# Kernel tuning notes

Hardware: AMD Instinct MI355X
Metric: run time of the kernel (lower is better)

The kernel has to match this reference:

```python
import jax, jax.numpy as jnp
import numpy as np

B, S, E, H = 2, 2048, 1024, 16
DH = E // H  # 64


def setup_inputs() -> dict:
    key = jax.random.key(0)
    ks = jax.random.split(key, 9)
    scale = 1.0 / np.sqrt(E)
    q = jax.random.normal(ks[0], (B, S, E), jnp.float32)
    k = jax.random.normal(ks[1], (B, S, E), jnp.float32)
    v = jax.random.normal(ks[2], (B, S, E), jnp.float32)
    Wq = jax.random.uniform(ks[3], (E, E), jnp.float32, -scale, scale)
    Wk = jax.random.uniform(ks[4], (E, E), jnp.float32, -scale, scale)
    Wv = jax.random.uniform(ks[5], (E, E), jnp.float32, -scale, scale)
    bq = jax.random.uniform(ks[6], (E,), jnp.float32, -scale, scale)
    bk = jax.random.uniform(ks[7], (E,), jnp.float32, -scale, scale)
    bv = jax.random.uniform(ks[8], (E,), jnp.float32, -scale, scale)
    # causal mask: True = masked. [b, s_q, s_k]
    causal = jnp.triu(jnp.ones((S, S), bool), k=1)
    mask = jnp.broadcast_to(causal, (B, S, S))
    return {"q": q, "k": k, "v": v, "Wq": Wq, "bq": bq, "Wk": Wk,
            "bk": bk, "Wv": Wv, "bv": bv, "mask": mask}


def reference(q, k, v, Wq, bq, Wk, bk, Wv, bv, mask):
    b, s_q, _ = q.shape
    s_k = k.shape[1]
    # NB: faithful to the original: .view(b, heads, s, -1) (no transpose)
    Q = (q @ Wq + bq).reshape(b, H, s_q, DH)
    K = (k @ Wk + bk).reshape(b, H, s_k, DH)
    V = (v @ Wv + bv).reshape(b, H, s_k, DH)
    scores = jnp.einsum('bhqd,bhkd->bhqk', Q, K) / jnp.sqrt(
        jnp.asarray(DH, Q.dtype))
    scores = jnp.where(mask[:, None, :, :], -jnp.inf, scores)
    attn = jax.nn.softmax(scores, axis=-1)
    out = jnp.einsum('bhqk,bhkd->bhqd', attn, V).reshape(b, s_q, -1)
    return out  # dropout p=0 / eval mode -> identity
```

## Files before the change

kernel.cpp:

```cpp
#include <hip/hip_runtime.h>

typedef unsigned short u16;
typedef __attribute__((ext_vector_type(8))) __bf16 bf16x8;
typedef __attribute__((ext_vector_type(4))) __bf16 bf16x4;
typedef __attribute__((ext_vector_type(4))) float f32x4;

#define MFMA(a, b, c) __builtin_amdgcn_mfma_f32_16x16x32_bf16((a), (b), (c), 0, 0, 0)
#define KSCALE 0.18033688011112042f

__device__ __forceinline__ void load_lds16(const void* g, void* l) {
  __builtin_amdgcn_global_load_lds(
      (__attribute__((address_space(1))) void*)(g),
      (__attribute__((address_space(3))) void*)(l), 16, 0, 0);
}

__device__ __forceinline__ float launder(float x, float lim) {
  return fminf(fmaxf(x, -lim), lim);
}

__global__ __launch_bounds__(256) void prep(
    const float* __restrict__ x0, const float* __restrict__ x1,
    const float* __restrict__ x2, const float* __restrict__ W0,
    const float* __restrict__ W1, const float* __restrict__ W2,
    __bf16* __restrict__ Xb, __bf16* __restrict__ WT) {
  __shared__ __bf16 tile[64][65];
  int bx = blockIdx.x;
  int t = threadIdx.x;
  if (bx < 3072) {
    int z = bx >> 10, blk = bx & 1023;
    const float* x = z == 0 ? x0 : (z == 1 ? x1 : x2);
    __bf16* o = Xb + (size_t)z * 4194304;
#pragma unroll
    for (int i = 0; i < 4; ++i) {
      size_t e = ((size_t)i * 262144 + (size_t)blk * 256 + t) * 4;
      f32x4 v = *(const f32x4*)&x[e];
      bf16x4 b = {(__bf16)v[0], (__bf16)v[1], (__bf16)v[2], (__bf16)v[3]};
      *(bf16x4*)&o[e] = b;
    }
  } else {
    int idx = bx - 3072;
    int z = idx >> 8, rest = idx & 255;
    const float* W = z == 0 ? W0 : (z == 1 ? W1 : W2);
    float sc = z == 0 ? KSCALE : 1.0f;
    __bf16* out = WT + (size_t)z * 1048576;
    int r0 = (rest >> 4) * 64, c0 = (rest & 15) * 64;
#pragma unroll
    for (int it = 0; it < 16; ++it) {
      int flat = it * 256 + t, r = flat >> 6, c = flat & 63;
      tile[c][r] = (__bf16)(W[(size_t)(r0 + r) * 1024 + c0 + c] * sc);
    }
    __syncthreads();
#pragma unroll
    for (int it = 0; it < 16; ++it) {
      int flat = it * 256 + t, r = flat >> 6, c = flat & 63;
      out[(size_t)(c0 + r) * 1024 + r0 + c] = tile[r][c];
    }
  }
}

__device__ __forceinline__ void pg_stage(
    const __bf16* __restrict__ A, const __bf16* __restrict__ Bm, int k0,
    __bf16* As, __bf16* Bs, int tid) {
#pragma unroll
  for (int r = 0; r < 2; ++r) {
    int flat = r * 256 + tid;
    int src = ((flat & 3) ^ ((flat >> 3) & 3)) * 8;
    load_lds16(A + (size_t)(flat >> 2) * 1024 + k0 + src, &As[flat * 8]);
  }
#pragma unroll
  for (int r = 0; r < 2; ++r) {
    int flat = r * 256 + tid;
    int src = ((flat & 3) ^ ((flat >> 3) & 3)) * 8;
    load_lds16(Bm + (size_t)(flat >> 2) * 1024 + k0 + src, &Bs[flat * 8]);
  }
}

__global__ __launch_bounds__(256, 3) void proj_gemm(
    const __bf16* __restrict__ Xb, const __bf16* __restrict__ WT,
    const float* __restrict__ bq, const float* __restrict__ bk,
    const float* __restrict__ bv, __bf16* __restrict__ QKV) {
  __shared__ __attribute__((aligned(16))) __bf16 As[3][4096];
  __shared__ __attribute__((aligned(16))) __bf16 Bs[3][4096];

  int tid = threadIdx.x;
  int lane = tid & 63, quad = lane >> 4, l16 = lane & 15;
  int w = tid >> 6;
  int wm = (w >> 1) * 64, wn = (w & 1) * 64;
  int sw = (l16 >> 1) & 3;
  int m0 = blockIdx.x * 128;
  int z = m0 >> 12;
  int n0 = blockIdx.y * 128;
  const __bf16* A = Xb + (size_t)m0 * 1024;
  const __bf16* Bm = WT + (size_t)z * 1048576 + (size_t)n0 * 1024;

  f32x4 zero4 = {0.f, 0.f, 0.f, 0.f};
  f32x4 acc[4][4];
#pragma unroll
  for (int i = 0; i < 4; ++i)
#pragma unroll
    for (int j = 0; j < 4; ++j) acc[i][j] = zero4;

  pg_stage(A, Bm, 0, As[0], Bs[0], tid);
  pg_stage(A, Bm, 32, As[1], Bs[1], tid);

  int cur = 0, stg = 2;
  for (int i = 0; i < 32; ++i) {
    if (i < 31) {
      asm volatile("s_waitcnt vmcnt(4)" ::: "memory");
    } else {
      asm volatile("s_waitcnt vmcnt(0)" ::: "memory");
    }
    __builtin_amdgcn_sched_barrier(0);
    __builtin_amdgcn_s_barrier();
    __builtin_amdgcn_sched_barrier(0);

    if (i < 30)
      pg_stage(A, Bm, (i + 2) * 32, As[stg], Bs[stg], tid);

    bf16x8 a[4], b[4];
#pragma unroll
    for (int mf = 0; mf < 4; ++mf)
      a[mf] = *(const bf16x8*)&As[cur][(wm + mf * 16 + l16) * 32 + ((quad ^ sw)) * 8];
#pragma unroll
    for (int nf = 0; nf < 4; ++nf)
      b[nf] = *(const bf16x8*)&Bs[cur][(wn + nf * 16 + l16) * 32 + ((quad ^ sw)) * 8];
#pragma unroll
    for (int mf = 0; mf < 4; ++mf)
#pragma unroll
      for (int nf = 0; nf < 4; ++nf) acc[mf][nf] = MFMA(a[mf], b[nf], acc[mf][nf]);

    cur = cur == 2 ? 0 : cur + 1;
    stg = stg == 2 ? 0 : stg + 1;
  }

  int mrow = m0 & 4095;
  const float* bp = z == 0 ? bq : (z == 1 ? bk : bv);
  float bsc = z == 0 ? KSCALE : 1.0f;
  __bf16* O = QKV + (size_t)z * 4194304;
#pragma unroll
  for (int nf = 0; nf < 4; ++nf) {
    int n = n0 + wn + nf * 16 + l16;
    float bb = bp[n] * bsc;
#pragma unroll
    for (int mf = 0; mf < 4; ++mf) {
#pragma unroll
      for (int r = 0; r < 4; ++r) {
        int m = mrow + wm + mf * 16 + quad * 4 + r;
        O[(size_t)m * 1024 + n] = (__bf16)launder(acc[mf][nf][r] + bb, 512.f);
      }
    }
  }
}

__global__ __launch_bounds__(256) void transpose_v(
    const u16* __restrict__ Vp, u16* __restrict__ Vt) {
  int bh = blockIdx.y, s0 = blockIdx.x * 64;
  __shared__ u16 tile[64][65];
  int t = threadIdx.x;
  const u16* src = Vp + (size_t)bh * 131072;
  u16* dst = Vt + (size_t)bh * 131072;
#pragma unroll
  for (int it = 0; it < 16; ++it) {
    int flat = it * 256 + t, r = flat >> 6, d = flat & 63;
    tile[d][r] = src[(size_t)(s0 + r) * 64 + d];
  }
  __syncthreads();
#pragma unroll
  for (int it = 0; it < 16; ++it) {
    int flat = it * 256 + t, d = flat >> 6, c = flat & 63;
    dst[(size_t)d * 2048 + s0 + c] = tile[d][c];
  }
}

__global__ __launch_bounds__(256, 4) void flash_attn(
    const __bf16* __restrict__ Qp, const __bf16* __restrict__ Kp,
    const __bf16* __restrict__ Vt, float* __restrict__ out) {
  int bh = blockIdx.x;
  int yy = blockIdx.y;
  int qt = (yy & 24) | (((yy >> 3) & 1) ? (7 - (yy & 7)) : (yy & 7));
  int jmax = qt;
  int t = threadIdx.x;
  int lane = t & 63, quad = lane >> 4, l16 = lane & 15;
  int w = t >> 6;
  int sw = (l16 >> 1) & 3;

  __shared__ __attribute__((aligned(16))) __bf16 Ks[2][4096];
  __shared__ __attribute__((aligned(16))) __bf16 Vs[2][4096];
  __shared__ __attribute__((aligned(16))) __bf16 Ps[4][1024];

  const __bf16* Qb = Qp + (size_t)bh * 131072;
  const __bf16* Kb = Kp + (size_t)bh * 131072;
  const __bf16* Vb = Vt + (size_t)bh * 131072;
  __bf16* Pw = Ps[w];

  int qb = qt * 64 + w * 16;

  bf16x8 qf[2], ones;
#pragma unroll
  for (int i = 0; i < 8; ++i) ones[i] = (__bf16)1.0f;
#pragma unroll
  for (int kk = 0; kk < 2; ++kk)
    qf[kk] = *(const bf16x8*)&Qb[(size_t)(qb + l16) * 64 + kk * 32 + quad * 8];

  f32x4 zero4 = {0.f, 0.f, 0.f, 0.f};
  f32x4 o[4], lacc = zero4;
#pragma unroll
  for (int nd = 0; nd < 4; ++nd) o[nd] = zero4;

  int kq_row[2], kq_off[2], v_d[2], v_off[2], v_kk[2];
#pragma unroll
  for (int p = 0; p < 2; ++p) {
    int c = p * 256 + t;
    int swz = ((c & 3) ^ ((c >> 3) & 3)) * 8;
    kq_row[p] = (c & 255) >> 2;
    kq_off[p] = (c >> 8) * 32 + swz;
    v_kk[p] = c >> 8;
    v_d[p] = (c & 255) >> 2;
    v_off[p] = swz;
  }

  bf16x8 pk[2], pv[2];
#pragma unroll
  for (int p = 0; p < 2; ++p) {
    pk[p] = *(const bf16x8*)&Kb[(size_t)kq_row[p] * 64 + kq_off[p]];
    pv[p] = *(const bf16x8*)&Vb[(size_t)v_d[p] * 2048 + v_kk[p] * 32 + v_off[p]];
  }
#pragma unroll
  for (int p = 0; p < 2; ++p) {
    int c = p * 256 + t;
    *(bf16x8*)&Ks[0][c * 8] = pk[p];
    *(bf16x8*)&Vs[0][c * 8] = pv[p];
  }
  if (jmax > 0) {
#pragma unroll
    for (int p = 0; p < 2; ++p) {
      pk[p] = *(const bf16x8*)&Kb[(size_t)(64 + kq_row[p]) * 64 + kq_off[p]];
      pv[p] = *(const bf16x8*)&Vb[(size_t)v_d[p] * 2048 + 64 + v_kk[p] * 32 + v_off[p]];
    }
  }
  __syncthreads();

  for (int j = 0; j <= jmax; ++j) {
    int cur = j & 1, nxt = cur ^ 1;

    if (j < jmax) {
#pragma unroll
      for (int p = 0; p < 2; ++p) {
        int c = p * 256 + t;
        *(bf16x8*)&Ks[nxt][c * 8] = pk[p];
        *(bf16x8*)&Vs[nxt][c * 8] = pv[p];
      }
      if (j + 1 < jmax) {
        int jn = (j + 2) * 64;
#pragma unroll
        for (int p = 0; p < 2; ++p) {
          pk[p] = *(const bf16x8*)&Kb[(size_t)(jn + kq_row[p]) * 64 + kq_off[p]];
          pv[p] = *(const bf16x8*)&Vb[(size_t)v_d[p] * 2048 + jn + v_kk[p] * 32 + v_off[p]];
        }
      }
    }

    f32x4 s[4];
#pragma unroll
    for (int nt = 0; nt < 4; ++nt) {
      bf16x8 k0 = *(const bf16x8*)&Ks[cur][(nt * 16 + l16) * 32 + (quad ^ sw) * 8];
      bf16x8 k1 = *(const bf16x8*)&Ks[cur][2048 + (nt * 16 + l16) * 32 + (quad ^ sw) * 8];
      f32x4 z = zero4;
      z = MFMA(k0, qf[0], z);
      z = MFMA(k1, qf[1], z);
      s[nt] = z;
    }

    if (j == jmax) {
      int qg = qb + l16;
#pragma unroll
      for (int nt = 0; nt < 4; ++nt) {
        int kg = j * 64 + nt * 16 + quad * 4;
#pragma unroll
        for (int r = 0; r < 4; ++r)
          if (kg + r > qg) s[nt][r] = -1e30f;
      }
    }
#pragma unroll
    for (int nt = 0; nt < 4; ++nt) {
      bf16x4 pb;
#pragma unroll
      for (int r = 0; r < 4; ++r)
        pb[r] = (__bf16)__builtin_amdgcn_exp2f(s[nt][r]);
      *(bf16x4*)&Pw[l16 * 64 + (((nt * 4 + quad) ^ (l16 * 2)) & 15) * 4] = pb;
    }
    {
      bf16x8 pf[2];
#pragma unroll
      for (int kk = 0; kk < 2; ++kk)
        pf[kk] = *(const bf16x8*)&Pw[l16 * 64 + (((kk * 8 + quad * 2) ^ (l16 * 2)) & 15) * 4];
#pragma unroll
      for (int kk = 0; kk < 2; ++kk) {
        lacc = MFMA(ones, pf[kk], lacc);
#pragma unroll
        for (int nd = 0; nd < 4; ++nd) {
          bf16x8 av = *(const bf16x8*)&Vs[cur][kk * 2048 + (nd * 16 + l16) * 32 + (quad ^ sw) * 8];
          o[nd] = MFMA(av, pf[kk], o[nd]);
        }
      }
    }
    __syncthreads();
  }

  {
    float inv = 1.f / lacc[0];
    int qg = qb + l16;
#pragma unroll
    for (int nd = 0; nd < 4; ++nd) {
      f32x4 a;
#pragma unroll
      for (int r = 0; r < 4; ++r) a[r] = launder(o[nd][r] * inv, 512.f);
      *(f32x4*)&out[(size_t)bh * 131072 + (size_t)qg * 64 + nd * 16 + quad * 4] = a;
    }
  }
}

extern "C" void kernel_launch(void* const* d_in, const int* in_sizes, int n_in,
                              void* d_out, int out_size, void* d_ws, size_t ws_size,
                              hipStream_t stream) {
  (void)in_sizes; (void)n_in; (void)out_size; (void)ws_size;
  const float* q  = (const float*)d_in[0];
  const float* k  = (const float*)d_in[1];
  const float* v  = (const float*)d_in[2];
  const float* Wq = (const float*)d_in[3];
  const float* bq = (const float*)d_in[4];
  const float* Wk = (const float*)d_in[5];
  const float* bk = (const float*)d_in[6];
  const float* Wv = (const float*)d_in[7];
  const float* bv = (const float*)d_in[8];

  __bf16* ws  = (__bf16*)d_ws;
  __bf16* WT  = ws;
  __bf16* QKV = ws + (size_t)3 * 1048576;
  __bf16* Qp  = QKV;
  __bf16* Kp  = QKV + (size_t)4194304;
  __bf16* Vp  = QKV + (size_t)2 * 4194304;
  __bf16* Xb  = QKV + (size_t)3 * 4194304;
  __bf16* Vtr = Xb;

  prep<<<dim3(3840), 256, 0, stream>>>(q, k, v, Wq, Wk, Wv, Xb, WT);
  proj_gemm<<<dim3(96, 8), 256, 0, stream>>>(Xb, WT, bq, bk, bv, QKV);
  transpose_v<<<dim3(32, 32), 256, 0, stream>>>((const u16*)Vp, (u16*)Vtr);
  flash_attn<<<dim3(32, 32), 256, 0, stream>>>(Qp, Kp, Vtr, (float*)d_out);
}
```

Before: 205.0 us.

## Fuse fp32-to-bf16 activation conversion into projection GEMM A-tile loads

Removes the separate activation conversion pass from the prep kernel. The projection GEMM now loads fp32 activations straight into registers, converts them to bf16 and writes them into a swizzled LDS tile. The weight tiles still arrive through direct global-to-LDS loads in a three-stage ring. This saves a full read and write of the bf16 activation copy and a kernel's worth of work, but the GEMM now reads twice the A bytes, uses more registers, and adds a second barrier per iteration.

```diff
diff --git a/kernel.cpp b/kernel.cpp
--- a/kernel.cpp
+++ b/kernel.cpp
@@ -18,69 +18,43 @@
   return fminf(fmaxf(x, -lim), lim);
 }
 
+__device__ __forceinline__ bf16x8 cvt8(f32x4 a, f32x4 b) {
+  bf16x8 r;
+  r[0] = (__bf16)a[0]; r[1] = (__bf16)a[1]; r[2] = (__bf16)a[2]; r[3] = (__bf16)a[3];
+  r[4] = (__bf16)b[0]; r[5] = (__bf16)b[1]; r[6] = (__bf16)b[2]; r[7] = (__bf16)b[3];
+  return r;
+}
+
 __global__ __launch_bounds__(256) void prep(
-    const float* __restrict__ x0, const float* __restrict__ x1,
-    const float* __restrict__ x2, const float* __restrict__ W0,
-    const float* __restrict__ W1, const float* __restrict__ W2,
-    __bf16* __restrict__ Xb, __bf16* __restrict__ WT) {
+    const float* __restrict__ W0, const float* __restrict__ W1,
+    const float* __restrict__ W2, __bf16* __restrict__ WT) {
   __shared__ __bf16 tile[64][65];
-  int bx = blockIdx.x;
+  int idx = blockIdx.x;
   int t = threadIdx.x;
-  if (bx < 3072) {
-    int z = bx >> 10, blk = bx & 1023;
-    const float* x = z == 0 ? x0 : (z == 1 ? x1 : x2);
-    __bf16* o = Xb + (size_t)z * 4194304;
-#pragma unroll
-    for (int i = 0; i < 4; ++i) {
-      size_t e = ((size_t)i * 262144 + (size_t)blk * 256 + t) * 4;
-      f32x4 v = *(const f32x4*)&x[e];
-      bf16x4 b = {(__bf16)v[0], (__bf16)v[1], (__bf16)v[2], (__bf16)v[3]};
-      *(bf16x4*)&o[e] = b;
-    }
-  } else {
-    int idx = bx - 3072;
-    int z = idx >> 8, rest = idx & 255;
-    const float* W = z == 0 ? W0 : (z == 1 ? W1 : W2);
-    float sc = z == 0 ? KSCALE : 1.0f;
-    __bf16* out = WT + (size_t)z * 1048576;
-    int r0 = (rest >> 4) * 64, c0 = (rest & 15) * 64;
-#pragma unroll
-    for (int it = 0; it < 16; ++it) {
-      int flat = it * 256 + t, r = flat >> 6, c = flat & 63;
-      tile[c][r] = (__bf16)(W[(size_t)(r0 + r) * 1024 + c0 + c] * sc);
-    }
-    __syncthreads();
-#pragma unroll
-    for (int it = 0; it < 16; ++it) {
-      int flat = it * 256 + t, r = flat >> 6, c = flat & 63;
-      out[(size_t)(c0 + r) * 1024 + r0 + c] = tile[r][c];
-    }
-  }
-}
-
-__device__ __forceinline__ void pg_stage(
-    const __bf16* __restrict__ A, const __bf16* __restrict__ Bm, int k0,
-    __bf16* As, __bf16* Bs, int tid) {
-#pragma unroll
-  for (int r = 0; r < 2; ++r) {
-    int flat = r * 256 + tid;
-    int src = ((flat & 3) ^ ((flat >> 3) & 3)) * 8;
-    load_lds16(A + (size_t)(flat >> 2) * 1024 + k0 + src, &As[flat * 8]);
-  }
-#pragma unroll
-  for (int r = 0; r < 2; ++r) {
-    int flat = r * 256 + tid;
-    int src = ((flat & 3) ^ ((flat >> 3) & 3)) * 8;
-    load_lds16(Bm + (size_t)(flat >> 2) * 1024 + k0 + src, &Bs[flat * 8]);
+  int z = idx >> 8, rest = idx & 255;
+  const float* W = z == 0 ? W0 : (z == 1 ? W1 : W2);
+  float sc = z == 0 ? KSCALE : 1.0f;
+  __bf16* out = WT + (size_t)z * 1048576;
+  int r0 = (rest >> 4) * 64, c0 = (rest & 15) * 64;
+#pragma unroll
+  for (int it = 0; it < 16; ++it) {
+    int flat = it * 256 + t, r = flat >> 6, c = flat & 63;
+    tile[c][r] = (__bf16)(W[(size_t)(r0 + r) * 1024 + c0 + c] * sc);
+  }
+  __syncthreads();
+#pragma unroll
+  for (int it = 0; it < 16; ++it) {
+    int flat = it * 256 + t, r = flat >> 6, c = flat & 63;
+    out[(size_t)(c0 + r) * 1024 + r0 + c] = tile[r][c];
   }
 }
 
 __global__ __launch_bounds__(256, 3) void proj_gemm(
-    const __bf16* __restrict__ Xb, const __bf16* __restrict__ WT,
+    const float* __restrict__ xq, const float* __restrict__ xk,
+    const float* __restrict__ xv, const __bf16* __restrict__ WT,
     const float* __restrict__ bq, const float* __restrict__ bk,
     const float* __restrict__ bv, __bf16* __restrict__ QKV) {
-  __shared__ __attribute__((aligned(16))) __bf16 As[3][4096];
-  __shared__ __attribute__((aligned(16))) __bf16 Bs[3][4096];
+  __shared__ __attribute__((aligned(16))) __bf16 shm[24576];
 
   int tid = threadIdx.x;
   int lane = tid & 63, quad = lane >> 4, l16 = lane & 15;
@@ -90,8 +64,15 @@
   int m0 = blockIdx.x * 128;
   int z = m0 >> 12;
   int n0 = blockIdx.y * 128;
-  const __bf16* A = Xb + (size_t)m0 * 1024;
+  int mrow = m0 & 4095;
+  const float* X = z == 0 ? xq : (z == 1 ? xk : xv);
   const __bf16* Bm = WT + (size_t)z * 1048576 + (size_t)n0 * 1024;
+
+  int r1 = tid >> 2, sp = tid & 3;
+  int g1 = sp ^ ((r1 >> 1) & 3);
+  int g2 = sp ^ (((64 + r1) >> 1) & 3);
+  const float* a1 = X + (size_t)(mrow + r1) * 1024 + g1 * 8;
+  const float* a2 = X + (size_t)(mrow + 64 + r1) * 1024 + g2 * 8;
 
   f32x4 zero4 = {0.f, 0.f, 0.f, 0.f};
   f32x4 acc[4][4];
@@ -100,40 +81,84 @@
 #pragma unroll
     for (int j = 0; j < 4; ++j) acc[i][j] = zero4;
 
-  pg_stage(A, Bm, 0, As[0], Bs[0], tid);
-  pg_stage(A, Bm, 32, As[1], Bs[1], tid);
+  f32x4 ra0[4], ra1[4];
+
+#define PG_ISSUE_A(k0, ra)                                   \
+  {                                                          \
+    ra[0] = *(const f32x4*)&a1[(k0)];                        \
+    ra[1] = *(const f32x4*)&a1[(k0) + 4];                    \
+    ra[2] = *(const f32x4*)&a2[(k0)];                        \
+    ra[3] = *(const f32x4*)&a2[(k0) + 4];                    \
+  }
+#define PG_ISSUE_B(k0, buf)                                                       \
+  {                                                                               \
+    _Pragma("unroll") for (int r = 0; r < 2; ++r) {                               \
+      int flat = r * 256 + tid;                                                   \
+      int src = ((flat & 3) ^ ((flat >> 3) & 3)) * 8;                             \
+      load_lds16(Bm + (size_t)(flat >> 2) * 1024 + (k0) + src,                    \
+                 &shm[12288 + (buf) * 4096 + flat * 8]);                          \
+    }                                                                             \
+  }
+#define PG_CVT_WRITE(ra, buf)                                                     \
+  {                                                                               \
+    *(bf16x8*)&shm[(buf) * 4096 + tid * 8] = cvt8(ra[0], ra[1]);                  \
+    *(bf16x8*)&shm[(buf) * 4096 + (tid + 256) * 8] = cvt8(ra[2], ra[3]);          \
+  }
+#define PG_COMPUTE(buf)                                                           \
+  {                                                                               \
+    bf16x8 a[4], b[4];                                                            \
+    _Pragma("unroll") for (int mf = 0; mf < 4; ++mf)                              \
+      a[mf] = *(const bf16x8*)&shm[(buf) * 4096 +                                 \
+                                   (wm + mf * 16 + l16) * 32 + (quad ^ sw) * 8];  \
+    _Pragma("unroll") for (int nf = 0; nf < 4; ++nf)                              \
+      b[nf] = *(const bf16x8*)&shm[12288 + (buf) * 4096 +                         \
+                                   (wn + nf * 16 + l16) * 32 + (quad ^ sw) * 8];  \
+    _Pragma("unroll") for (int mf = 0; mf < 4; ++mf)                              \
+      _Pragma("unroll") for (int nf = 0; nf < 4; ++nf)                            \
+        acc[mf][nf] = MFMA(a[mf], b[nf], acc[mf][nf]);                            \
+  }
+#define PG_BAR1()                              \
+  asm volatile("s_waitcnt lgkmcnt(0)" ::: "memory"); \
+  __builtin_amdgcn_sched_barrier(0);           \
+  __builtin_amdgcn_s_barrier();                \
+  __builtin_amdgcn_sched_barrier(0);
+#define PG_BAR2()                              \
+  __builtin_amdgcn_sched_barrier(0);           \
+  __builtin_amdgcn_s_barrier();                \
+  __builtin_amdgcn_sched_barrier(0);
+
+  PG_ISSUE_A(0, ra0);
+  PG_ISSUE_B(0, 0);
+  PG_ISSUE_A(32, ra1);
+  PG_ISSUE_B(32, 1);
+  asm volatile("s_waitcnt vmcnt(8)" ::: "memory");
+  PG_CVT_WRITE(ra0, 0);
 
   int cur = 0, stg = 2;
+#pragma unroll 2
   for (int i = 0; i < 32; ++i) {
-    if (i < 31) {
-      asm volatile("s_waitcnt vmcnt(4)" ::: "memory");
+    if (i < 30) {
+      if ((i & 1) == 0) { PG_ISSUE_A((i + 2) * 32, ra0); }
+      else              { PG_ISSUE_A((i + 2) * 32, ra1); }
+      PG_ISSUE_B((i + 2) * 32, stg);
+      asm volatile("s_waitcnt vmcnt(6)" ::: "memory");
+    } else if (i == 30) {
+      asm volatile("s_waitcnt vmcnt(2)" ::: "memory");
     } else {
       asm volatile("s_waitcnt vmcnt(0)" ::: "memory");
     }
-    __builtin_amdgcn_sched_barrier(0);
-    __builtin_amdgcn_s_barrier();
-    __builtin_amdgcn_sched_barrier(0);
-
-    if (i < 30)
-      pg_stage(A, Bm, (i + 2) * 32, As[stg], Bs[stg], tid);
-
-    bf16x8 a[4], b[4];
-#pragma unroll
-    for (int mf = 0; mf < 4; ++mf)
-      a[mf] = *(const bf16x8*)&As[cur][(wm + mf * 16 + l16) * 32 + ((quad ^ sw)) * 8];
-#pragma unroll
-    for (int nf = 0; nf < 4; ++nf)
-      b[nf] = *(const bf16x8*)&Bs[cur][(wn + nf * 16 + l16) * 32 + ((quad ^ sw)) * 8];
-#pragma unroll
-    for (int mf = 0; mf < 4; ++mf)
-#pragma unroll
-      for (int nf = 0; nf < 4; ++nf) acc[mf][nf] = MFMA(a[mf], b[nf], acc[mf][nf]);
-
+    if (i < 31) {
+      int wb = stg == 0 ? 2 : stg - 1;
+      if ((i & 1) == 0) { PG_CVT_WRITE(ra1, wb); }
+      else              { PG_CVT_WRITE(ra0, wb); }
+    }
+    PG_BAR1();
+    PG_COMPUTE(cur);
+    PG_BAR2();
     cur = cur == 2 ? 0 : cur + 1;
     stg = stg == 2 ? 0 : stg + 1;
   }
 
-  int mrow = m0 & 4095;
   const float* bp = z == 0 ? bq : (z == 1 ? bk : bv);
   float bsc = z == 0 ? KSCALE : 1.0f;
   __bf16* O = QKV + (size_t)z * 4194304;
@@ -340,11 +365,10 @@
   __bf16* Qp  = QKV;
   __bf16* Kp  = QKV + (size_t)4194304;
   __bf16* Vp  = QKV + (size_t)2 * 4194304;
-  __bf16* Xb  = QKV + (size_t)3 * 4194304;
-  __bf16* Vtr = Xb;
-
-  prep<<<dim3(3840), 256, 0, stream>>>(q, k, v, Wq, Wk, Wv, Xb, WT);
-  proj_gemm<<<dim3(96, 8), 256, 0, stream>>>(Xb, WT, bq, bk, bv, QKV);
+  __bf16* Vtr = QKV + (size_t)3 * 4194304;
+
+  prep<<<dim3(768), 256, 0, stream>>>(Wq, Wk, Wv, WT);
+  proj_gemm<<<dim3(96, 8), 256, 0, stream>>>(q, k, v, WT, bq, bk, bv, QKV);
   transpose_v<<<dim3(32, 32), 256, 0, stream>>>((const u16*)Vp, (u16*)Vtr);
   flash_attn<<<dim3(32, 32), 256, 0, stream>>>(Qp, Kp, Vtr, (float*)d_out);
 }
```

Result: no change. 204.6 us (-0.2%).
